# Performance work log

Measured on AMD Instinct MI355X. Metric: run time of the kernel, lower is better.

The kernel has to match this reference:

```python
import jax, jax.numpy as jnp
import numpy as np

B, N, C, H = 8, 4096, 768, 32
D = C // H  # head_dim = 24
EPS = 1e-12


def _l2norm(t):
    # F.normalize(dim=-1): t / max(||t||_2, eps)
    n = jnp.sqrt(jnp.sum(t * t, axis=-1, keepdims=True))
    return t / jnp.maximum(n, EPS)


def setup_inputs() -> dict:
    key = jax.random.key(0)
    ks = jax.random.split(key, 6)
    s_in = 1.0 / np.sqrt(C)
    return {
        "x": jax.random.normal(ks[0], (B, N, C), dtype=jnp.float32),
        "W_qkv": jax.random.uniform(ks[1], (C, 3 * C), jnp.float32, -s_in, s_in),
        "b_qkv": jax.random.uniform(ks[2], (3 * C,), jnp.float32, -s_in, s_in),
        "temperature": jnp.ones((H, 1, 1), dtype=jnp.float32),
        "W_proj": jax.random.uniform(ks[3], (C, C), jnp.float32, -s_in, s_in),
        "b_proj": jax.random.uniform(ks[4], (C,), jnp.float32, -s_in, s_in),
    }


def reference(x, W_qkv, b_qkv, temperature, W_proj, b_proj):
    b, n, c = x.shape
    qkv = x @ W_qkv + b_qkv                                  # (B,N,3C)
    qkv = qkv.reshape(b, n, 3, H, D).transpose(2, 0, 3, 1, 4)  # (3,B,H,N,D)
    q, k, v = qkv[0], qkv[1], qkv[2]                         # (B,H,N,D)
    q = jnp.swapaxes(q, -1, -2)                              # (B,H,D,N)
    k = jnp.swapaxes(k, -1, -2)
    v = jnp.swapaxes(v, -1, -2)
    q = _l2norm(q)                                           # normalize over N
    k = _l2norm(k)
    attn = jnp.einsum('bhdn,bhen->bhde', q, k) * temperature  # (B,H,D,D)
    attn = jax.nn.softmax(attn, axis=-1)
    y = jnp.einsum('bhde,bhen->bhdn', attn, v)               # (B,H,D,N)
    # Faithful to torch: (1,B,H,D,N).transpose(1,2).reshape(B,N,C)
    # == (H,B,D,N) flattened row-major into (B,N,C)
    y = jnp.transpose(y, (1, 0, 2, 3)).reshape(b, n, c)
    return y @ W_proj + b_proj
```

## Files before the change

kernel.cpp:

```cpp
#include <hip/hip_runtime.h>
#include <hip/hip_bf16.h>


#define DEVI __device__ __forceinline__

typedef __attribute__((ext_vector_type(8))) short bf16x8;
typedef __attribute__((ext_vector_type(4))) float f32x4;
typedef unsigned int u32;
typedef unsigned short u16;

DEVI u16 f2bf(float f) {
  union { float f; u32 u; } x; x.f = f;
  u32 r = x.u + 0x7FFFu + ((x.u >> 16) & 1u);
  return (u16)(r >> 16);
}

DEVI void gload_lds16(const void* g, void* l) {
  __builtin_amdgcn_global_load_lds((__attribute__((address_space(1))) void*)g,
                                   (__attribute__((address_space(3))) void*)l, 16, 0, 0);
}

__global__ __launch_bounds__(256) void cvt_kernel(const float* __restrict__ in,
                                                  u16* __restrict__ out, int n8) {
  int i = blockIdx.x * 256 + threadIdx.x;
  if (i >= n8) return;
  long o = (long)i * 8;
  float4 a = *(const float4*)(in + o);
  float4 b = *(const float4*)(in + o + 4);
  uint4 v;
  v.x = f2bf(a.x) | ((u32)f2bf(a.y) << 16);
  v.y = f2bf(a.z) | ((u32)f2bf(a.w) << 16);
  v.z = f2bf(b.x) | ((u32)f2bf(b.y) << 16);
  v.w = f2bf(b.z) | ((u32)f2bf(b.w) << 16);
  *(uint4*)(out + o) = v;
}

__global__ __launch_bounds__(256) void transpose_cvt(const float* __restrict__ W,
                                                     u16* __restrict__ Wt, int K, int N) {
  __shared__ float tile[32][33];
  int n0 = blockIdx.x * 32, k0 = blockIdx.y * 32;
  int tx = threadIdx.x, ty = threadIdx.y;
  #pragma unroll
  for (int i = 0; i < 4; ++i)
    tile[ty + 8 * i][tx] = W[(long)(k0 + ty + 8 * i) * N + n0 + tx];
  __syncthreads();
  #pragma unroll
  for (int i = 0; i < 4; ++i)
    Wt[(long)(n0 + ty + 8 * i) * K + k0 + tx] = f2bf(tile[tx][ty + 8 * i]);
}

#define STAGE_T(ktile, slot)                                                   \
  { gload_lds16(Ag + soffA + (ktile) * 32, lds + (slot) * 8192 + sdst);        \
    _Pragma("unroll") for (int j_ = 0; j_ < 2; ++j_)                           \
      gload_lds16(Bg + soffB[j_] + (ktile) * 32,                               \
                  lds + 24576 + (slot) * 16384 + j_ * 8192 + sdst); }

template<int NT, int BF16_OUT>
__global__ __launch_bounds__(512, 4) void gemm2b_kernel(
    const u16* __restrict__ A, const u16* __restrict__ Bt,
    const float* __restrict__ bias, void* __restrict__ Cout,
    int M, int N) {
  constexpr int K = NT * 32;
  __shared__ __attribute__((aligned(128))) char lds[73728];

  int nbx = N >> 8;
  int nwg = gridDim.x;
  int bid = blockIdx.x;
  bid = (bid & 7) * (nwg >> 3) + (bid >> 3);
  int bx = bid % nbx, by = bid / nbx;

  int t = threadIdx.x;
  int w = t >> 6, l = t & 63;
  int wr = w >> 2, wc = w & 3;
  int l16 = l & 15, l4 = l >> 4;

  int cbb = (l4 * 16) ^ ((l16 & 8) << 2);
  int pA0 = (wr * 64 + l16) * 64 + cbb;
  int pB0 = (wc * 64 + l16) * 64 + cbb;

  int pa = t * 16;
  int la = pa ^ (((pa >> 9) & 1) << 5);
  int soffA = (la >> 6) * K + ((la & 63) >> 1);
  int soffB[2];
  #pragma unroll
  for (int j = 0; j < 2; ++j) {
    int p = (j * 512 + t) * 16;
    int lb = p ^ (((p >> 9) & 1) << 5);
    soffB[j] = (lb >> 6) * K + ((lb & 63) >> 1);
  }

  const u16* Ag = A + (long)by * 128 * K;
  const u16* Bg = Bt + (long)bx * 256 * K;
  int sdst = w * 1024;

  f32x4 acc[4][4] = {};

  STAGE_T(0, 0);
  STAGE_T(1, 1);

  #pragma unroll
  for (int kt = 0; kt < NT; ++kt) {
    int rs = kt % 3;
    if (kt + 2 < NT) {
      STAGE_T(kt + 2, (kt + 2) % 3);
      asm volatile("s_waitcnt vmcnt(6)" ::: "memory");
    } else if (kt + 2 == NT) {
      asm volatile("s_waitcnt vmcnt(3)" ::: "memory");
    } else {
      asm volatile("s_waitcnt vmcnt(0)" ::: "memory");
    }
    __builtin_amdgcn_sched_barrier(0);
    __builtin_amdgcn_s_barrier();
    __builtin_amdgcn_sched_barrier(0);

    bf16x8 aF[4], bF[4];
    #pragma unroll
    for (int mi = 0; mi < 4; ++mi)
      aF[mi] = *(const bf16x8*)(lds + rs * 8192 + mi * 1024 + pA0);
    #pragma unroll
    for (int n = 0; n < 4; ++n)
      bF[n] = *(const bf16x8*)(lds + 24576 + rs * 16384 + n * 1024 + pB0);

    __builtin_amdgcn_s_setprio(1);
    #pragma unroll
    for (int mi = 0; mi < 4; ++mi)
      #pragma unroll
      for (int n = 0; n < 4; ++n)
        acc[mi][n] = __builtin_amdgcn_mfma_f32_16x16x32_bf16(aF[mi], bF[n], acc[mi][n], 0, 0, 0);
    __builtin_amdgcn_s_setprio(0);
    __builtin_amdgcn_s_barrier();
    __builtin_amdgcn_sched_barrier(0);
  }

  #pragma unroll
  for (int mi = 0; mi < 4; ++mi) {
    int row0 = by * 128 + wr * 64 + mi * 16 + l4 * 4;
    #pragma unroll
    for (int n = 0; n < 4; ++n) {
      int col = bx * 256 + wc * 64 + n * 16 + l16;
      float bv = bias[col];
      #pragma unroll
      for (int j = 0; j < 4; ++j) {
        long idx = (long)(row0 + j) * N + col;
        float v = acc[mi][n][j] + bv;
        if (BF16_OUT) ((u16*)Cout)[idx] = f2bf(v);
        else          __builtin_nontemporal_store(v, (float*)Cout + idx);
      }
    }
  }
}

#define PFQK(nc, rq, rk)                                                       \
  { long cb = (long)(nc) * 589824;                                             \
    _Pragma("unroll") for (int i = 0; i < 3; ++i) {                            \
      rq[i] = *(const uint4*)(qbase + cb + offI[i]);                           \
      rk[i] = *(const uint4*)(kbase + cb + offI[i]); } }

#define WRQK(rq, rk)                                                           \
  { _Pragma("unroll") for (int i = 0; i < 3; ++i) {                            \
      const u32* pq = (const u32*)&rq[i];                                      \
      const u32* pk = (const u32*)&rk[i];                                      \
      _Pragma("unroll") for (int j = 0; j < 4; ++j) {                          \
        int d = sI[i] * 8 + 2 * j;                                             \
        qt[d][nI[i]] = (u16)pq[j]; qt[d + 1][nI[i]] = (u16)(pq[j] >> 16);      \
        kt[d][nI[i]] = (u16)pk[j]; kt[d + 1][nI[i]] = (u16)(pk[j] >> 16); } } }

#define GRAM8                                                                  \
  { _Pragma("unroll") for (int ks = 0; ks < 8; ++ks) {                         \
      int koff = ks * 32 + l4 * 8;                                             \
      bf16x8 qa = *(const bf16x8*)&qt[fm * 16 + l16][koff];                    \
      bf16x8 qb = *(const bf16x8*)&qt[fn * 16 + l16][koff];                    \
      bf16x8 ka = *(const bf16x8*)&kt[fm * 16 + l16][koff];                    \
      bf16x8 kb = *(const bf16x8*)&kt[fn * 16 + l16][koff];                    \
      accG = __builtin_amdgcn_mfma_f32_16x16x32_bf16(qa, kb, accG, 0, 0, 0);   \
      accQ = __builtin_amdgcn_mfma_f32_16x16x32_bf16(qa, qb, accQ, 0, 0, 0);   \
      accK = __builtin_amdgcn_mfma_f32_16x16x32_bf16(ka, kb, accK, 0, 0, 0); } }

__global__ __launch_bounds__(256) void gram_kernel(const u16* __restrict__ qkv,
                                                   float* __restrict__ gram) {
  __shared__ u16 qt[32][280];
  __shared__ u16 kt[32][280];

  int bid = blockIdx.x;
  int bh = bid >> 2, s = bid & 3;
  int b = bh >> 5, h = bh & 31;
  int t = threadIdx.x;
  int w = t >> 6, l = t & 63;
  int l16 = l & 15, l4 = l >> 4;
  int fm = w >> 1, fn = w & 1;

  for (int i = t; i < 32 * 280; i += 256) { qt[0][i] = 0; kt[0][i] = 0; }

  int nI[3], sI[3], offI[3];
  #pragma unroll
  for (int i = 0; i < 3; ++i) {
    int idx = t + 256 * i;
    nI[i] = idx / 3; sI[i] = idx % 3;
    offI[i] = nI[i] * 2304 + sI[i] * 8;
  }

  f32x4 accG = {}, accQ = {}, accK = {};
  const u16* qbase = qkv + (long)b * 4096 * 2304 + h * 24;
  const u16* kbase = qbase + 768;
  int c0 = s * 4;

  uint4 rq[3], rk[3];
  PFQK(c0, rq, rk);
  __syncthreads();

  #pragma unroll
  for (int c = 0; c < 4; ++c) {
    WRQK(rq, rk);
    __syncthreads();
    if (c + 1 < 4) PFQK(c0 + c + 1, rq, rk);
    GRAM8;
    __syncthreads();
  }

  float* gb = gram + (long)(bh * 4 + s) * 3072;
  int row = fm * 16 + l4 * 4, col = fn * 16 + l16;
  #pragma unroll
  for (int j = 0; j < 4; ++j) {
    gb[(row + j) * 32 + col] = accG[j];
    gb[1024 + (row + j) * 32 + col] = accQ[j];
    gb[2048 + (row + j) * 32 + col] = accK[j];
  }
}

__global__ __launch_bounds__(32) void softmax_kernel(const float* __restrict__ gram,
                                                     const float* __restrict__ temperature,
                                                     u16* __restrict__ attnb) {
  int bh = blockIdx.x;
  int h = bh & 31;
  int d = threadIdx.x;
  u16* ab = attnb + bh * 1024;
  if (d < 24) {
    const float* gb = gram + (long)bh * 12288;
    float nq2 = 0.f, row[24], nk2[24];
    #pragma unroll
    for (int e = 0; e < 24; ++e) { row[e] = 0.f; nk2[e] = 0.f; }
    #pragma unroll
    for (int s = 0; s < 4; ++s) {
      const float* gs = gb + s * 3072;
      nq2 += gs[1024 + d * 33];
      #pragma unroll
      for (int e = 0; e < 24; ++e) {
        row[e] += gs[d * 32 + e];
        nk2[e] += gs[2048 + e * 33];
      }
    }
    float nq = fmaxf(sqrtf(fmaxf(nq2, 0.f)), 1e-12f);
    float tmp = temperature[h];
    float mx = -1e30f;
    #pragma unroll
    for (int e = 0; e < 24; ++e) {
      float nk = fmaxf(sqrtf(fmaxf(nk2[e], 0.f)), 1e-12f);
      row[e] = row[e] / (nq * nk) * tmp;
      mx = fmaxf(mx, row[e]);
    }
    float ssum = 0.f;
    #pragma unroll
    for (int e = 0; e < 24; ++e) { row[e] = __expf(row[e] - mx); ssum += row[e]; }
    float inv = 1.f / ssum;
    #pragma unroll
    for (int e = 0; e < 24; ++e) ab[d * 32 + e] = f2bf(row[e] * inv);
    #pragma unroll
    for (int e = 24; e < 32; ++e) ab[d * 32 + e] = 0;
  } else {
    #pragma unroll
    for (int e = 0; e < 32; ++e) ab[d * 32 + e] = 0;
  }
}

__global__ __launch_bounds__(256) void pv_kernel(const u16* __restrict__ qkv,
                                                 const u16* __restrict__ attnb,
                                                 u16* __restrict__ yout) {
  __shared__ u16 vl[256][40];
  int bid = blockIdx.x;
  int bh = bid >> 4, c = bid & 15;
  int b = bh >> 5, h = bh & 31;
  int t = threadIdx.x;
  int w = t >> 6, l = t & 63;
  int l16 = l & 15, l4 = l >> 4;

  for (int i = t; i < 5120; i += 256) ((u32*)vl)[i] = 0;

  const u16* ab = attnb + bh * 1024;
  bf16x8 af0 = *(const bf16x8*)(ab + l16 * 32 + l4 * 8);
  bf16x8 af1 = *(const bf16x8*)(ab + (16 + l16) * 32 + l4 * 8);

  const u16* vbase = qkv + (long)b * 4096 * 2304 + h * 24 + 1536;
  uint4 rv[3];
  int nI[3], sI[3];
  #pragma unroll
  for (int i = 0; i < 3; ++i) {
    int idx = t + 256 * i;
    nI[i] = idx / 3; sI[i] = idx % 3;
    rv[i] = *(const uint4*)(vbase + (long)c * 589824 + nI[i] * 2304 + sI[i] * 8);
  }
  __syncthreads();
  #pragma unroll
  for (int i = 0; i < 3; ++i) *(uint4*)&vl[nI[i]][sI[i] * 8] = rv[i];
  __syncthreads();

  u16* ybase = yout + (long)(h * 8 + b) * 24 * 4096;
  int n0 = c * 256;
  f32x4 z = {};
  #pragma unroll
  for (int fnn = 0; fnn < 4; ++fnn) {
    int ncol = w * 64 + fnn * 16 + l16;
    bf16x8 bv = *(const bf16x8*)&vl[ncol][l4 * 8];
    f32x4 y0 = __builtin_amdgcn_mfma_f32_16x16x32_bf16(af0, bv, z, 0, 0, 0);
    f32x4 y1 = __builtin_amdgcn_mfma_f32_16x16x32_bf16(af1, bv, z, 0, 0, 0);
    int gn = n0 + ncol;
    #pragma unroll
    for (int j = 0; j < 4; ++j) {
      int d0 = l4 * 4 + j;
      ybase[(long)d0 * 4096 + gn] = f2bf(y0[j]);
      int d1 = 16 + d0;
      if (d1 < 24) ybase[(long)d1 * 4096 + gn] = f2bf(y1[j]);
    }
  }
}

extern "C" void kernel_launch(void* const* d_in, const int* in_sizes, int n_in,
                              void* d_out, int out_size, void* d_ws, size_t ws_size,
                              hipStream_t stream) {
  const float* x     = (const float*)d_in[0];
  const float* Wqkv  = (const float*)d_in[1];
  const float* bqkv  = (const float*)d_in[2];
  const float* temp  = (const float*)d_in[3];
  const float* Wproj = (const float*)d_in[4];
  const float* bproj = (const float*)d_in[5];
  float* out = (float*)d_out;

  char* ws = (char*)d_ws;
  u16*   xb    = (u16*)(ws);
  float* gram  = (float*)(ws);
  u16*   y     = (u16*)(ws);
  u16*   wqt   = (u16*)(ws + 50331648);
  u16*   attnb = (u16*)(ws + 50331648);
  u16*   wpt   = (u16*)(ws + 53870592);
  u16*   qkv   = (u16*)(ws + 55050240);

  cvt_kernel<<<12288, 256, 0, stream>>>(x, xb, 3145728);
  transpose_cvt<<<dim3(72, 24), dim3(32, 8), 0, stream>>>(Wqkv, wqt, 768, 2304);
  transpose_cvt<<<dim3(24, 24), dim3(32, 8), 0, stream>>>(Wproj, wpt, 768, 768);
  gemm2b_kernel<24, 1><<<2304, 512, 0, stream>>>(xb, wqt, bqkv, qkv, 32768, 2304);
  gram_kernel<<<1024, 256, 0, stream>>>(qkv, gram);
  softmax_kernel<<<256, 32, 0, stream>>>(gram, temp, attnb);
  pv_kernel<<<4096, 256, 0, stream>>>(qkv, attnb, y);
  gemm2b_kernel<24, 0><<<768, 512, 0, stream>>>(y, wpt, bproj, out, 32768, 768);
}
```

Baseline: 299.0 us.

## Fuse fp32-to-bf16 conversion of x into QKV GEMM; retile projection GEMM

The standalone x conversion kernel is removed. The QKV GEMM now loads fp32 x into registers, converts it with packed bf16 conversion instructions and writes the A tile to LDS itself, pipelined alongside the async B loads. This saves a full write and re-read of the bf16 copy of x, at the cost of more registers and lower occupancy (launch bounds 2). The output projection GEMM switches to a 128x128 tile kernel with 256 threads and 1536 workgroups, giving better CU fill for N=768.

```diff
diff --git a/kernel.cpp b/kernel.cpp
--- a/kernel.cpp
+++ b/kernel.cpp
@@ -6,6 +6,7 @@
 
 typedef __attribute__((ext_vector_type(8))) short bf16x8;
 typedef __attribute__((ext_vector_type(4))) float f32x4;
+typedef __attribute__((ext_vector_type(4))) unsigned int u32x4;
 typedef unsigned int u32;
 typedef unsigned short u16;
 
@@ -15,24 +16,15 @@
   return (u16)(r >> 16);
 }
 
+DEVI u32 cvtpk(float a, float b) {
+  u32 r;
+  asm("v_cvt_pk_bf16_f32 %0, %1, %2" : "=v"(r) : "v"(a), "v"(b));
+  return r;
+}
+
 DEVI void gload_lds16(const void* g, void* l) {
   __builtin_amdgcn_global_load_lds((__attribute__((address_space(1))) void*)g,
                                    (__attribute__((address_space(3))) void*)l, 16, 0, 0);
-}
-
-__global__ __launch_bounds__(256) void cvt_kernel(const float* __restrict__ in,
-                                                  u16* __restrict__ out, int n8) {
-  int i = blockIdx.x * 256 + threadIdx.x;
-  if (i >= n8) return;
-  long o = (long)i * 8;
-  float4 a = *(const float4*)(in + o);
-  float4 b = *(const float4*)(in + o + 4);
-  uint4 v;
-  v.x = f2bf(a.x) | ((u32)f2bf(a.y) << 16);
-  v.y = f2bf(a.z) | ((u32)f2bf(a.w) << 16);
-  v.z = f2bf(b.x) | ((u32)f2bf(b.y) << 16);
-  v.w = f2bf(b.z) | ((u32)f2bf(b.w) << 16);
-  *(uint4*)(out + o) = v;
 }
 
 __global__ __launch_bounds__(256) void transpose_cvt(const float* __restrict__ W,
@@ -49,17 +41,10 @@
     Wt[(long)(n0 + ty + 8 * i) * K + k0 + tx] = f2bf(tile[tx][ty + 8 * i]);
 }
 
-#define STAGE_T(ktile, slot)                                                   \
-  { gload_lds16(Ag + soffA + (ktile) * 32, lds + (slot) * 8192 + sdst);        \
-    _Pragma("unroll") for (int j_ = 0; j_ < 2; ++j_)                           \
-      gload_lds16(Bg + soffB[j_] + (ktile) * 32,                               \
-                  lds + 24576 + (slot) * 16384 + j_ * 8192 + sdst); }
-
-template<int NT, int BF16_OUT>
-__global__ __launch_bounds__(512, 4) void gemm2b_kernel(
-    const u16* __restrict__ A, const u16* __restrict__ Bt,
-    const float* __restrict__ bias, void* __restrict__ Cout,
-    int M, int N) {
+template<int NT>
+__global__ __launch_bounds__(512, 2) void gemm_k1f_kernel(
+    const float* __restrict__ X, const u16* __restrict__ Bt,
+    const float* __restrict__ bias, u16* __restrict__ Cout, int N) {
   constexpr int K = NT * 32;
   __shared__ __attribute__((aligned(128))) char lds[73728];
 
@@ -89,26 +74,56 @@
     soffB[j] = (lb >> 6) * K + ((lb & 63) >> 1);
   }
 
-  const u16* Ag = A + (long)by * 128 * K;
+  const float* Ag = X + (long)by * 128 * K;
   const u16* Bg = Bt + (long)bx * 256 * K;
   int sdst = w * 1024;
 
   f32x4 acc[4][4] = {};
-
-  STAGE_T(0, 0);
-  STAGE_T(1, 1);
+  f32x4 rC0, rC1, rN0, rN1;
+
+  rC0 = *(const f32x4*)(Ag + soffA);
+  rC1 = *(const f32x4*)(Ag + soffA + 4);
+  #pragma unroll
+  for (int j = 0; j < 2; ++j)
+    gload_lds16(Bg + soffB[j], lds + 24576 + j * 8192 + sdst);
+  rN0 = *(const f32x4*)(Ag + soffA + 32);
+  rN1 = *(const f32x4*)(Ag + soffA + 36);
+  #pragma unroll
+  for (int j = 0; j < 2; ++j)
+    gload_lds16(Bg + soffB[j] + 32, lds + 24576 + 16384 + j * 8192 + sdst);
+  asm volatile("s_waitcnt vmcnt(6)" ::: "memory");
+  {
+    u32x4 wv;
+    wv[0] = cvtpk(rC0[0], rC0[1]); wv[1] = cvtpk(rC0[2], rC0[3]);
+    wv[2] = cvtpk(rC1[0], rC1[1]); wv[3] = cvtpk(rC1[2], rC1[3]);
+    *(u32x4*)(lds + t * 16) = wv;
+  }
+  rC0 = rN0; rC1 = rN1;
 
   #pragma unroll
   for (int kt = 0; kt < NT; ++kt) {
     int rs = kt % 3;
     if (kt + 2 < NT) {
-      STAGE_T(kt + 2, (kt + 2) % 3);
-      asm volatile("s_waitcnt vmcnt(6)" ::: "memory");
+      rN0 = *(const f32x4*)(Ag + soffA + (kt + 2) * 32);
+      rN1 = *(const f32x4*)(Ag + soffA + (kt + 2) * 32 + 4);
+      #pragma unroll
+      for (int j = 0; j < 2; ++j)
+        gload_lds16(Bg + soffB[j] + (kt + 2) * 32,
+                    lds + 24576 + ((kt + 2) % 3) * 16384 + j * 8192 + sdst);
+      asm volatile("s_waitcnt vmcnt(4)" ::: "memory");
     } else if (kt + 2 == NT) {
-      asm volatile("s_waitcnt vmcnt(3)" ::: "memory");
+      asm volatile("s_waitcnt vmcnt(2)" ::: "memory");
     } else {
       asm volatile("s_waitcnt vmcnt(0)" ::: "memory");
     }
+    if (kt + 1 < NT) {
+      u32x4 wv;
+      wv[0] = cvtpk(rC0[0], rC0[1]); wv[1] = cvtpk(rC0[2], rC0[3]);
+      wv[2] = cvtpk(rC1[0], rC1[1]); wv[3] = cvtpk(rC1[2], rC1[3]);
+      *(u32x4*)(lds + ((kt + 1) % 3) * 8192 + t * 16) = wv;
+      rC0 = rN0; rC1 = rN1;
+    }
+    asm volatile("s_waitcnt lgkmcnt(0)" ::: "memory");
     __builtin_amdgcn_sched_barrier(0);
     __builtin_amdgcn_s_barrier();
     __builtin_amdgcn_sched_barrier(0);
@@ -142,9 +157,105 @@
       #pragma unroll
       for (int j = 0; j < 4; ++j) {
         long idx = (long)(row0 + j) * N + col;
-        float v = acc[mi][n][j] + bv;
-        if (BF16_OUT) ((u16*)Cout)[idx] = f2bf(v);
-        else          __builtin_nontemporal_store(v, (float*)Cout + idx);
+        Cout[idx] = f2bf(acc[mi][n][j] + bv);
+      }
+    }
+  }
+}
+
+#define STAGE3(ktile, slot)                                                    \
+  { _Pragma("unroll") for (int j_ = 0; j_ < 2; ++j_) {                         \
+      gload_lds16(Ag + soffA[j_] + (ktile) * 32,                               \
+                  lds + (slot) * 8192 + j_ * 4096 + sdst);                     \
+      gload_lds16(Bg + soffB[j_] + (ktile) * 32,                               \
+                  lds + 24576 + (slot) * 8192 + j_ * 4096 + sdst); } }
+
+template<int NT>
+__global__ __launch_bounds__(256, 3) void gemm3c_kernel(
+    const u16* __restrict__ A, const u16* __restrict__ Bt,
+    const float* __restrict__ bias, float* __restrict__ Cout,
+    int M, int N) {
+  constexpr int K = NT * 32;
+  __shared__ __attribute__((aligned(128))) char lds[49152];
+
+  int nbx = N >> 7;
+  int nwg = gridDim.x;
+  int bid = blockIdx.x;
+  bid = (bid & 7) * (nwg >> 3) + (bid >> 3);
+  int bx = bid % nbx, by = bid / nbx;
+
+  int t = threadIdx.x;
+  int w = t >> 6, l = t & 63;
+  int wr = w >> 1, wc = w & 1;
+  int l16 = l & 15, l4 = l >> 4;
+
+  int cbb = (l4 * 16) ^ ((l16 & 8) << 2);
+  int pA0 = (wr * 64 + l16) * 64 + cbb;
+  int pB0 = (wc * 64 + l16) * 64 + cbb;
+
+  int soffA[2], soffB[2];
+  #pragma unroll
+  for (int j = 0; j < 2; ++j) {
+    int p = (j * 256 + t) * 16;
+    int lb = p ^ (((p >> 9) & 1) << 5);
+    soffA[j] = (lb >> 6) * K + ((lb & 63) >> 1);
+    soffB[j] = soffA[j];
+  }
+
+  const u16* Ag = A + (long)by * 128 * K;
+  const u16* Bg = Bt + (long)bx * 128 * K;
+  int sdst = w * 1024;
+
+  f32x4 acc[4][4] = {};
+
+  STAGE3(0, 0);
+  STAGE3(1, 1);
+
+  #pragma unroll
+  for (int kt = 0; kt < NT; ++kt) {
+    int rs = kt % 3;
+    if (kt + 2 < NT) {
+      STAGE3(kt + 2, (kt + 2) % 3);
+      asm volatile("s_waitcnt vmcnt(8)" ::: "memory");
+    } else if (kt + 2 == NT) {
+      asm volatile("s_waitcnt vmcnt(4)" ::: "memory");
+    } else {
+      asm volatile("s_waitcnt vmcnt(0)" ::: "memory");
+    }
+    __builtin_amdgcn_sched_barrier(0);
+    __builtin_amdgcn_s_barrier();
+    __builtin_amdgcn_sched_barrier(0);
+
+    bf16x8 aF[4], bF[4];
+    #pragma unroll
+    for (int mi = 0; mi < 4; ++mi)
+      aF[mi] = *(const bf16x8*)(lds + rs * 8192 + mi * 1024 + pA0);
+    #pragma unroll
+    for (int n = 0; n < 4; ++n)
+      bF[n] = *(const bf16x8*)(lds + 24576 + rs * 8192 + n * 1024 + pB0);
+
+    __builtin_amdgcn_s_setprio(1);
+    #pragma unroll
+    for (int mi = 0; mi < 4; ++mi)
+      #pragma unroll
+      for (int n = 0; n < 4; ++n)
+        acc[mi][n] = __builtin_amdgcn_mfma_f32_16x16x32_bf16(aF[mi], bF[n], acc[mi][n], 0, 0, 0);
+    __builtin_amdgcn_s_setprio(0);
+    __builtin_amdgcn_s_barrier();
+    __builtin_amdgcn_sched_barrier(0);
+  }
+
+  #pragma unroll
+  for (int mi = 0; mi < 4; ++mi) {
+    int row0 = by * 128 + wr * 64 + mi * 16 + l4 * 4;
+    #pragma unroll
+    for (int n = 0; n < 4; ++n) {
+      int col = bx * 128 + wc * 64 + n * 16 + l16;
+      float bv = bias[col];
+      #pragma unroll
+      for (int j = 0; j < 4; ++j) {
+        long idx = (long)(row0 + j) * N + col;
+        __builtin_nontemporal_store(acc[mi][n][j] + bv, Cout + idx);
       }
     }
   }
@@ -335,7 +446,6 @@
   float* out = (float*)d_out;
 
   char* ws = (char*)d_ws;
-  u16*   xb    = (u16*)(ws);
   float* gram  = (float*)(ws);
   u16*   y     = (u16*)(ws);
   u16*   wqt   = (u16*)(ws + 50331648);
@@ -343,12 +453,11 @@
   u16*   wpt   = (u16*)(ws + 53870592);
   u16*   qkv   = (u16*)(ws + 55050240);
 
-  cvt_kernel<<<12288, 256, 0, stream>>>(x, xb, 3145728);
   transpose_cvt<<<dim3(72, 24), dim3(32, 8), 0, stream>>>(Wqkv, wqt, 768, 2304);
   transpose_cvt<<<dim3(24, 24), dim3(32, 8), 0, stream>>>(Wproj, wpt, 768, 768);
-  gemm2b_kernel<24, 1><<<2304, 512, 0, stream>>>(xb, wqt, bqkv, qkv, 32768, 2304);
+  gemm_k1f_kernel<24><<<2304, 512, 0, stream>>>(x, wqt, bqkv, qkv, 2304);
   gram_kernel<<<1024, 256, 0, stream>>>(qkv, gram);
   softmax_kernel<<<256, 32, 0, stream>>>(gram, temp, attnb);
   pv_kernel<<<4096, 256, 0, stream>>>(qkv, attnb, y);
-  gemm2b_kernel<24, 0><<<768, 512, 0, stream>>>(y, wpt, bproj, out, 32768, 768);
-}
+  gemm3c_kernel<24><<<1536, 256, 0, stream>>>(y, wpt, bproj, out, 32768, 768);
+}
```

New measurement: 329.3 us. 1.1x slower.

## Load GEMM B operand directly into registers, bypassing LDS staging

Applied to the files above, without the earlier changes.

The GEMM kernel no longer stages the B (weight) tile through LDS. Each wave now loads its own B fragments straight from global memory into a double-buffered register set, prefetched two k-tiles ahead. The A tile keeps the three-slot LDS pipeline, so the LDS footprint drops from 72KB to 24KB, which frees LDS for occupancy and removes the B-tile LDS writes and reads. The cost is that each B fragment is now fetched from global memory by every wave row that uses it, the reads are strided by row, and the extra register buffers raise VGPR pressure under the existing launch bounds.

```diff
diff --git a/kernel.cpp b/kernel.cpp
--- a/kernel.cpp
+++ b/kernel.cpp
@@ -49,19 +49,13 @@
     Wt[(long)(n0 + ty + 8 * i) * K + k0 + tx] = f2bf(tile[tx][ty + 8 * i]);
 }
 
-#define STAGE_T(ktile, slot)                                                   \
-  { gload_lds16(Ag + soffA + (ktile) * 32, lds + (slot) * 8192 + sdst);        \
-    _Pragma("unroll") for (int j_ = 0; j_ < 2; ++j_)                           \
-      gload_lds16(Bg + soffB[j_] + (ktile) * 32,                               \
-                  lds + 24576 + (slot) * 16384 + j_ * 8192 + sdst); }
-
 template<int NT, int BF16_OUT>
-__global__ __launch_bounds__(512, 4) void gemm2b_kernel(
+__global__ __launch_bounds__(512, 4) void gemm_bd_kernel(
     const u16* __restrict__ A, const u16* __restrict__ Bt,
     const float* __restrict__ bias, void* __restrict__ Cout,
     int M, int N) {
   constexpr int K = NT * 32;
-  __shared__ __attribute__((aligned(128))) char lds[73728];
+  __shared__ __attribute__((aligned(128))) char lds[24576];
 
   int nbx = N >> 8;
   int nwg = gridDim.x;
@@ -76,36 +70,40 @@
 
   int cbb = (l4 * 16) ^ ((l16 & 8) << 2);
   int pA0 = (wr * 64 + l16) * 64 + cbb;
-  int pB0 = (wc * 64 + l16) * 64 + cbb;
 
   int pa = t * 16;
   int la = pa ^ (((pa >> 9) & 1) << 5);
   int soffA = (la >> 6) * K + ((la & 63) >> 1);
-  int soffB[2];
-  #pragma unroll
-  for (int j = 0; j < 2; ++j) {
-    int p = (j * 512 + t) * 16;
-    int lb = p ^ (((p >> 9) & 1) << 5);
-    soffB[j] = (lb >> 6) * K + ((lb & 63) >> 1);
-  }
 
   const u16* Ag = A + (long)by * 128 * K;
-  const u16* Bg = Bt + (long)bx * 256 * K;
   int sdst = w * 1024;
 
+  const u16* Bq[4];
+  #pragma unroll
+  for (int n = 0; n < 4; ++n)
+    Bq[n] = Bt + (long)(bx * 256 + wc * 64 + n * 16 + l16) * K + l4 * 8;
+
   f32x4 acc[4][4] = {};
-
-  STAGE_T(0, 0);
-  STAGE_T(1, 1);
+  bf16x8 bR[2][4];
+
+  gload_lds16(Ag + soffA, lds + sdst);
+  #pragma unroll
+  for (int n = 0; n < 4; ++n) bR[0][n] = *(const bf16x8*)(Bq[n]);
+  gload_lds16(Ag + soffA + 32, lds + 8192 + sdst);
+  #pragma unroll
+  for (int n = 0; n < 4; ++n) bR[1][n] = *(const bf16x8*)(Bq[n] + 32);
+  asm volatile("s_waitcnt vmcnt(5)" ::: "memory");
+  __builtin_amdgcn_s_barrier();
 
   #pragma unroll
   for (int kt = 0; kt < NT; ++kt) {
     int rs = kt % 3;
-    if (kt + 2 < NT) {
-      STAGE_T(kt + 2, (kt + 2) % 3);
+    int ci = kt & 1;
+    if (kt < NT - 2) {
+      gload_lds16(Ag + soffA + (kt + 2) * 32, lds + ((kt + 2) % 3) * 8192 + sdst);
       asm volatile("s_waitcnt vmcnt(6)" ::: "memory");
-    } else if (kt + 2 == NT) {
-      asm volatile("s_waitcnt vmcnt(3)" ::: "memory");
+    } else if (kt == NT - 2) {
+      asm volatile("s_waitcnt vmcnt(5)" ::: "memory");
     } else {
       asm volatile("s_waitcnt vmcnt(0)" ::: "memory");
     }
@@ -113,21 +111,24 @@
     __builtin_amdgcn_s_barrier();
     __builtin_amdgcn_sched_barrier(0);
 
-    bf16x8 aF[4], bF[4];
+    bf16x8 aF[4];
     #pragma unroll
     for (int mi = 0; mi < 4; ++mi)
       aF[mi] = *(const bf16x8*)(lds + rs * 8192 + mi * 1024 + pA0);
-    #pragma unroll
-    for (int n = 0; n < 4; ++n)
-      bF[n] = *(const bf16x8*)(lds + 24576 + rs * 16384 + n * 1024 + pB0);
 
     __builtin_amdgcn_s_setprio(1);
     #pragma unroll
     for (int mi = 0; mi < 4; ++mi)
       #pragma unroll
       for (int n = 0; n < 4; ++n)
-        acc[mi][n] = __builtin_amdgcn_mfma_f32_16x16x32_bf16(aF[mi], bF[n], acc[mi][n], 0, 0, 0);
+        acc[mi][n] = __builtin_amdgcn_mfma_f32_16x16x32_bf16(aF[mi], bR[ci][n], acc[mi][n], 0, 0, 0);
     __builtin_amdgcn_s_setprio(0);
+
+    if (kt < NT - 2) {
+      #pragma unroll
+      for (int n = 0; n < 4; ++n)
+        bR[ci][n] = *(const bf16x8*)(Bq[n] + (kt + 2) * 32);
+    }
     __builtin_amdgcn_s_barrier();
     __builtin_amdgcn_sched_barrier(0);
   }
@@ -346,9 +347,9 @@
   cvt_kernel<<<12288, 256, 0, stream>>>(x, xb, 3145728);
   transpose_cvt<<<dim3(72, 24), dim3(32, 8), 0, stream>>>(Wqkv, wqt, 768, 2304);
   transpose_cvt<<<dim3(24, 24), dim3(32, 8), 0, stream>>>(Wproj, wpt, 768, 768);
-  gemm2b_kernel<24, 1><<<2304, 512, 0, stream>>>(xb, wqt, bqkv, qkv, 32768, 2304);
+  gemm_bd_kernel<24, 1><<<2304, 512, 0, stream>>>(xb, wqt, bqkv, qkv, 32768, 2304);
   gram_kernel<<<1024, 256, 0, stream>>>(qkv, gram);
   softmax_kernel<<<256, 32, 0, stream>>>(gram, temp, attnb);
   pv_kernel<<<4096, 256, 0, stream>>>(qkv, attnb, y);
-  gemm2b_kernel<24, 0><<<768, 512, 0, stream>>>(y, wpt, bproj, out, 32768, 768);
-}
+  gemm_bd_kernel<24, 0><<<768, 512, 0, stream>>>(y, wpt, bproj, out, 32768, 768);
+}
```

New measurement: 446.7 us. +49.4%, slower.

## Shrink GEMM tile to 128x128 with 256 threads and merge weight transposes

Applied to the files above, without the earlier changes.

Both projection GEMMs now use a 128x128 output tile computed by 4 waves of 256 threads instead of a 128x256 tile over 8 waves, with 48KB of LDS and 3 blocks per CU as the launch-bound occupancy hint. This doubles the grid size, which is meant to improve load balance and wave-level concurrency across the CUs, especially for the smaller 768-wide output projection. The two weight transpose-convert launches are also merged into one kernel to save a launch. The cost is less operand reuse per tile, so more global and LDS traffic for each MFMA.

```diff
diff --git a/kernel.cpp b/kernel.cpp
--- a/kernel.cpp
+++ b/kernel.cpp
@@ -35,10 +35,16 @@
   *(uint4*)(out + o) = v;
 }
 
-__global__ __launch_bounds__(256) void transpose_cvt(const float* __restrict__ W,
-                                                     u16* __restrict__ Wt, int K, int N) {
+__global__ __launch_bounds__(256) void transpose_cvt2(const float* __restrict__ Wq,
+                                                      u16* __restrict__ Wqt,
+                                                      const float* __restrict__ Wp,
+                                                      u16* __restrict__ Wpt) {
   __shared__ float tile[32][33];
-  int n0 = blockIdx.x * 32, k0 = blockIdx.y * 32;
+  int bx = blockIdx.x;
+  const float* W; u16* Wt; int N, n0;
+  if (bx < 72) { W = Wq; Wt = Wqt; N = 2304; n0 = bx * 32; }
+  else         { W = Wp; Wt = Wpt; N = 768;  n0 = (bx - 72) * 32; }
+  int k0 = blockIdx.y * 32;
   int tx = threadIdx.x, ty = threadIdx.y;
   #pragma unroll
   for (int i = 0; i < 4; ++i)
@@ -46,24 +52,25 @@
   __syncthreads();
   #pragma unroll
   for (int i = 0; i < 4; ++i)
-    Wt[(long)(n0 + ty + 8 * i) * K + k0 + tx] = f2bf(tile[tx][ty + 8 * i]);
-}
-
-#define STAGE_T(ktile, slot)                                                   \
-  { gload_lds16(Ag + soffA + (ktile) * 32, lds + (slot) * 8192 + sdst);        \
-    _Pragma("unroll") for (int j_ = 0; j_ < 2; ++j_)                           \
+    Wt[(long)(n0 + ty + 8 * i) * 768 + k0 + tx] = f2bf(tile[tx][ty + 8 * i]);
+}
+
+#define STAGE3(ktile, slot)                                                    \
+  { _Pragma("unroll") for (int j_ = 0; j_ < 2; ++j_) {                         \
+      gload_lds16(Ag + soffA[j_] + (ktile) * 32,                               \
+                  lds + (slot) * 8192 + j_ * 4096 + sdst);                     \
       gload_lds16(Bg + soffB[j_] + (ktile) * 32,                               \
-                  lds + 24576 + (slot) * 16384 + j_ * 8192 + sdst); }
+                  lds + 24576 + (slot) * 8192 + j_ * 4096 + sdst); } }
 
 template<int NT, int BF16_OUT>
-__global__ __launch_bounds__(512, 4) void gemm2b_kernel(
+__global__ __launch_bounds__(256, 3) void gemm3c_kernel(
     const u16* __restrict__ A, const u16* __restrict__ Bt,
     const float* __restrict__ bias, void* __restrict__ Cout,
     int M, int N) {
   constexpr int K = NT * 32;
-  __shared__ __attribute__((aligned(128))) char lds[73728];
-
-  int nbx = N >> 8;
+  __shared__ __attribute__((aligned(128))) char lds[49152];
+
+  int nbx = N >> 7;
   int nwg = gridDim.x;
   int bid = blockIdx.x;
   bid = (bid & 7) * (nwg >> 3) + (bid >> 3);
@@ -71,41 +78,39 @@
 
   int t = threadIdx.x;
   int w = t >> 6, l = t & 63;
-  int wr = w >> 2, wc = w & 3;
+  int wr = w >> 1, wc = w & 1;
   int l16 = l & 15, l4 = l >> 4;
 
   int cbb = (l4 * 16) ^ ((l16 & 8) << 2);
   int pA0 = (wr * 64 + l16) * 64 + cbb;
   int pB0 = (wc * 64 + l16) * 64 + cbb;
 
-  int pa = t * 16;
-  int la = pa ^ (((pa >> 9) & 1) << 5);
-  int soffA = (la >> 6) * K + ((la & 63) >> 1);
-  int soffB[2];
+  int soffA[2], soffB[2];
   #pragma unroll
   for (int j = 0; j < 2; ++j) {
-    int p = (j * 512 + t) * 16;
+    int p = (j * 256 + t) * 16;
     int lb = p ^ (((p >> 9) & 1) << 5);
-    soffB[j] = (lb >> 6) * K + ((lb & 63) >> 1);
+    soffA[j] = (lb >> 6) * K + ((lb & 63) >> 1);
+    soffB[j] = soffA[j];
   }
 
   const u16* Ag = A + (long)by * 128 * K;
-  const u16* Bg = Bt + (long)bx * 256 * K;
+  const u16* Bg = Bt + (long)bx * 128 * K;
   int sdst = w * 1024;
 
   f32x4 acc[4][4] = {};
 
-  STAGE_T(0, 0);
-  STAGE_T(1, 1);
+  STAGE3(0, 0);
+  STAGE3(1, 1);
 
   #pragma unroll
   for (int kt = 0; kt < NT; ++kt) {
     int rs = kt % 3;
     if (kt + 2 < NT) {
-      STAGE_T(kt + 2, (kt + 2) % 3);
-      asm volatile("s_waitcnt vmcnt(6)" ::: "memory");
+      STAGE3(kt + 2, (kt + 2) % 3);
+      asm volatile("s_waitcnt vmcnt(8)" ::: "memory");
     } else if (kt + 2 == NT) {
-      asm volatile("s_waitcnt vmcnt(3)" ::: "memory");
+      asm volatile("s_waitcnt vmcnt(4)" ::: "memory");
     } else {
       asm volatile("s_waitcnt vmcnt(0)" ::: "memory");
     }
@@ -119,7 +124,7 @@
       aF[mi] = *(const bf16x8*)(lds + rs * 8192 + mi * 1024 + pA0);
     #pragma unroll
     for (int n = 0; n < 4; ++n)
-      bF[n] = *(const bf16x8*)(lds + 24576 + rs * 16384 + n * 1024 + pB0);
+      bF[n] = *(const bf16x8*)(lds + 24576 + rs * 8192 + n * 1024 + pB0);
 
     __builtin_amdgcn_s_setprio(1);
     #pragma unroll
@@ -137,7 +142,7 @@
     int row0 = by * 128 + wr * 64 + mi * 16 + l4 * 4;
     #pragma unroll
     for (int n = 0; n < 4; ++n) {
-      int col = bx * 256 + wc * 64 + n * 16 + l16;
+      int col = bx * 128 + wc * 64 + n * 16 + l16;
       float bv = bias[col];
       #pragma unroll
       for (int j = 0; j < 4; ++j) {
@@ -344,11 +349,10 @@
   u16*   qkv   = (u16*)(ws + 55050240);
 
   cvt_kernel<<<12288, 256, 0, stream>>>(x, xb, 3145728);
-  transpose_cvt<<<dim3(72, 24), dim3(32, 8), 0, stream>>>(Wqkv, wqt, 768, 2304);
-  transpose_cvt<<<dim3(24, 24), dim3(32, 8), 0, stream>>>(Wproj, wpt, 768, 768);
-  gemm2b_kernel<24, 1><<<2304, 512, 0, stream>>>(xb, wqt, bqkv, qkv, 32768, 2304);
+  transpose_cvt2<<<dim3(96, 24), dim3(32, 8), 0, stream>>>(Wqkv, wqt, Wproj, wpt);
+  gemm3c_kernel<24, 1><<<4608, 256, 0, stream>>>(xb, wqt, bqkv, qkv, 32768, 2304);
   gram_kernel<<<1024, 256, 0, stream>>>(qkv, gram);
   softmax_kernel<<<256, 32, 0, stream>>>(gram, temp, attnb);
   pv_kernel<<<4096, 256, 0, stream>>>(qkv, attnb, y);
-  gemm2b_kernel<24, 0><<<768, 512, 0, stream>>>(y, wpt, bproj, out, 32768, 768);
-}
+  gemm3c_kernel<24, 0><<<1536, 256, 0, stream>>>(y, wpt, bproj, out, 32768, 768);
+}
```

Measured after the change: 316.8 us. 6.0% more time.
